# Kernel optimization log

Measured on AMD Instinct MI355X. Metric: run time of the kernel, lower is better.

Reference implementation:

```python
import math
import jax, jax.numpy as jnp
import numpy as np

PROB_SPARSE_FACTOR = 0.4


def setup_inputs() -> dict:
    key = jax.random.key(0)
    kq, kk, kv = jax.random.split(key, 3)
    B, H, T, S, D = 2, 16, 2048, 2048, 64
    q = jax.random.normal(kq, (B, H, T, D), dtype=jnp.float32)
    k = jax.random.normal(kk, (B, H, S, D), dtype=jnp.float32)
    v = jax.random.normal(kv, (B, H, S, D), dtype=jnp.float32)
    return {"q": q, "k": k, "v": v}


def reference(q, k, v):
    B, H, T, D = q.shape
    S = k.shape[2]
    scaling = 1.0 / math.sqrt(D)
    # Informer-style top-u query count (static, derived from shapes)
    u = max(int(min(PROB_SPARSE_FACTOR * math.log(S), T * 0.5)), int(T * 0.3))

    # KLD scoring over full attention approximation: [B,H,T,S]
    attn_approx = jnp.einsum("bhtd,bhsd->bhts", q * scaling, k)
    attn_approx = jnp.clip(attn_approx, -50.0, 50.0)
    attn_approx = attn_approx - jnp.max(attn_approx, axis=-1, keepdims=True)
    sm = jax.nn.softmax(attn_approx, axis=-1)
    log_uniform = math.log(S)
    kl_score = jnp.sum(sm * (jnp.log(sm + 1e-10) + log_uniform), axis=-1)  # [B,H,T]

    # Select top-u most informative queries per (b,h)
    _, topk_idx = jax.lax.top_k(kl_score, u)  # [B,H,u]

    # Sparse attention only for selected queries
    q_red = jnp.take_along_axis(q, topk_idx[..., None], axis=2)  # [B,H,u,D]
    scores = jnp.einsum("bhud,bhsd->bhus", q_red, k) * scaling
    scores = jnp.clip(scores, -50.0, 50.0)
    scores = scores - jnp.max(scores, axis=-1, keepdims=True)
    w = jax.nn.softmax(scores, axis=-1)
    w = jnp.clip(w, 1e-9, 1.0)
    out_red = jnp.einsum("bhus,bhsd->bhud", w, v)  # [B,H,u,D]

    # Scatter reduced outputs back into a zero-initialized full output
    b_i = jnp.arange(B)[:, None, None]
    h_i = jnp.arange(H)[None, :, None]
    out = jnp.zeros_like(q).at[b_i, h_i, topk_idx].set(out_red)
    return out
```

## Files before the change

kernel.cpp:

```cpp
#include <hip/hip_runtime.h>
#include <math.h>

#define T_DIM 2048
#define S_DIM 2048
#define D_DIM 64
#define BH_DIM 32
#define U_SEL 614
#define QROWS 48
#define LOG_S_D 7.624618986159398
#define LOG2E_F 1.4426950408889634f
#define LN2_D 0.6931471805599453
#define SCL_Q (0.125f * LOG2E_F)

typedef __attribute__((ext_vector_type(8))) short bf16x8;
typedef __attribute__((ext_vector_type(4))) short bf16x4;
typedef __attribute__((ext_vector_type(4))) float f32x4;

__device__ __forceinline__ unsigned short bf16_rne(float x) {
  unsigned u = __float_as_uint(x);
  u += 0x7FFF + ((u >> 16) & 1);
  return (unsigned short)(u >> 16);
}
__device__ __forceinline__ float bf16_to_f(unsigned short h) {
  return __uint_as_float(((unsigned)h) << 16);
}
#if defined(__has_builtin)
#if __has_builtin(__builtin_amdgcn_exp2f)
#define EXP2_HW(x) __builtin_amdgcn_exp2f(x)
#endif
#endif
#ifndef EXP2_HW
#define EXP2_HW(x) exp2f(x)
#endif

#define GLD_LDS16(g, l)                                                        \
  __builtin_amdgcn_global_load_lds(                                            \
      (const __attribute__((address_space(1))) unsigned int*)(const void*)(g), \
      (__attribute__((address_space(3))) unsigned int*)(void*)(l), 16, 0, 0)

__device__ __forceinline__ void stage_img16(const unsigned short* __restrict__ g,
                                            unsigned short* l, int lane, int w) {
#pragma unroll
  for (int it = 0; it < 4; ++it) {
    const int chunk = it * 4 + w;
    GLD_LDS16((const char*)g + chunk * 1024 + lane * 16, (char*)l + chunk * 1024);
  }
}
__device__ __forceinline__ void stage_img8(const unsigned short* __restrict__ g,
                                           unsigned short* l, int lane, int w) {
#pragma unroll
  for (int it = 0; it < 2; ++it) {
    const int chunk = it * 4 + w;
    GLD_LDS16((const char*)g + chunk * 1024 + lane * 16, (char*)l + chunk * 1024);
  }
}

__device__ __forceinline__ bf16x8 ldfrag_sw(const unsigned short* buf, int row, int chunk) {
  return *(const bf16x8*)(buf + (row << 6) + (((chunk) ^ (row & 7)) << 3));
}
__device__ __forceinline__ bf16x8 ldfrag_k128(const unsigned short* buf, int row, int chunk) {
  return *(const bf16x8*)(buf + ((row >> 6) << 12) + ((row & 63) << 6) +
                          (((chunk) ^ (row & 7)) << 3));
}

__global__ __launch_bounds__(256) void convert_kernel(
    const float* __restrict__ kin, const float* __restrict__ vin,
    const float* __restrict__ qin, unsigned short* __restrict__ kimg,
    unsigned short* __restrict__ vt_g, unsigned short* __restrict__ qimg,
    float* __restrict__ out) {
  __shared__ float vld[128][65];
  const int jb = blockIdx.x;
  const int tid = threadIdx.x;
  if (jb < 2048) {
    const bool isq = jb >= 1024;
    const int jj = jb & 1023;
    const int bh = jj >> 5, tl = jj & 31;
    const float* src = (isq ? qin : kin) + ((size_t)bh * 2048 + tl * 64) * 64;
    unsigned short* dst = (isq ? qimg : kimg) + (size_t)(bh * 32 + tl) * 8192;
    const float scl = isq ? SCL_Q : 1.0f;
#pragma unroll
    for (int g = 0; g < 2; ++g) {
      const int flat = g * 256 + tid;
      const int r = flat >> 3, c = flat & 7;
      const float4 f0 = *(const float4*)(src + r * 64 + c * 8);
      const float4 f1 = *(const float4*)(src + r * 64 + c * 8 + 4);
      const float xs[8] = {f0.x, f0.y, f0.z, f0.w, f1.x, f1.y, f1.z, f1.w};
      bf16x8 hv, lv;
#pragma unroll
      for (int j = 0; j < 8; ++j) {
        const float x = xs[j] * scl;
        const unsigned short h = bf16_rne(x);
        hv[j] = (short)h;
        lv[j] = (short)bf16_rne(x - bf16_to_f(h));
      }
      const int base = (r << 6) + ((c ^ (r & 7)) << 3);
      *(bf16x8*)(dst + base) = hv;
      *(bf16x8*)(dst + 4096 + base) = lv;
    }
  } else if (jb < 2560) {
    const int jv = jb - 2048;
    const int bh = jv >> 4, tl = jv & 15;
    const float* src = vin + ((size_t)bh * 2048 + tl * 128) * 64;
#pragma unroll
    for (int g = 0; g < 8; ++g) {
      const int f = g * 256 + tid;
      const int r = f >> 4, c4 = f & 15;
      const float4 x = *(const float4*)(src + r * 64 + c4 * 4);
      vld[r][c4 * 4 + 0] = x.x;
      vld[r][c4 * 4 + 1] = x.y;
      vld[r][c4 * 4 + 2] = x.z;
      vld[r][c4 * 4 + 3] = x.w;
    }
    __syncthreads();
    unsigned short* dst = vt_g + (size_t)(bh * 16 + tl) * 8192;
#pragma unroll
    for (int g = 0; g < 4; ++g) {
      const int oc = g * 256 + tid;
      const int d = oc >> 4, cc = oc & 15;
      bf16x8 hv;
#pragma unroll
      for (int j = 0; j < 8; ++j) hv[j] = (short)bf16_rne(vld[cc * 8 + j][d]);
      *(bf16x8*)(dst + (d << 7) + (((cc ^ (d & 15))) << 3)) = hv;
    }
  } else {
    float4* o4 = (float4*)out;
    const size_t b = (size_t)(jb - 2560);
#pragma unroll
    for (int g = 0; g < 8; ++g)
      o4[b * 2048 + g * 256 + tid] = make_float4(0.f, 0.f, 0.f, 0.f);
  }
}

__global__ __launch_bounds__(256, 2) void kl_score_mfma(
    const unsigned short* __restrict__ qimg, const unsigned short* __restrict__ kimg,
    float2* __restrict__ zw) {
  __shared__ __align__(16) unsigned short lbuf[2][8192];
  const int b = blockIdx.x;
  const int bh = b & 31;
  const int tt = (b >> 5) & 15;
  const int shalf = b >> 9;
  const int tid = threadIdx.x;
  const int lane = tid & 63, w = tid >> 6, quad = lane >> 4, l15 = lane & 15;
  const unsigned short* qb = qimg + (size_t)(bh * 32 + tt * 2) * 8192;
  const unsigned short* kb = kimg + (size_t)bh * (32 * 8192);
  const int tg0 = shalf * 16;

  stage_img16(qb, &lbuf[0][0], lane, w);
  stage_img16(qb + 8192, &lbuf[1][0], lane, w);
  __syncthreads();

  bf16x8 ah[2][2], al[2][2];
#pragma unroll
  for (int rt = 0; rt < 2; ++rt) {
    const int row = w * 32 + rt * 16 + l15;
    const unsigned short* lb = &lbuf[row >> 6][0];
    const int r64 = row & 63;
#pragma unroll
    for (int kc = 0; kc < 2; ++kc) {
      const int off = (r64 << 6) + (((kc * 4 + quad) ^ (r64 & 7)) << 3);
      ah[rt][kc] = *(const bf16x8*)(lb + off);
      al[rt][kc] = *(const bf16x8*)(lb + 4096 + off);
    }
  }
  __syncthreads();

  stage_img16(kb + (size_t)tg0 * 8192, &lbuf[0][0], lane, w);
  __syncthreads();

  float Zf[8], Wf[8];
#pragma unroll
  for (int i = 0; i < 8; ++i) { Zf[i] = 0.f; Wf[i] = 0.f; }

  for (int t = 0; t < 16; ++t) {
    if (t < 15)
      stage_img16(kb + (size_t)(tg0 + t + 1) * 8192, &lbuf[(t + 1) & 1][0], lane, w);
    const unsigned short* cb = &lbuf[t & 1][0];

    f32x4 acc[2][4];
#pragma unroll
    for (int rt = 0; rt < 2; ++rt)
#pragma unroll
      for (int ct = 0; ct < 4; ++ct) acc[rt][ct] = (f32x4){0.f, 0.f, 0.f, 0.f};

#pragma unroll
    for (int ct = 0; ct < 4; ++ct) {
      const int srow = ct * 16 + l15;
      const bf16x8 bh0 = ldfrag_sw(cb, srow, quad);
      const bf16x8 bl0 = ldfrag_sw(cb + 4096, srow, quad);
      const bf16x8 bh1 = ldfrag_sw(cb, srow, 4 + quad);
      const bf16x8 bl1 = ldfrag_sw(cb + 4096, srow, 4 + quad);
#pragma unroll
      for (int rt = 0; rt < 2; ++rt) {
        f32x4 c = acc[rt][ct];
        c = __builtin_amdgcn_mfma_f32_16x16x32_bf16(ah[rt][0], bh0, c, 0, 0, 0);
        c = __builtin_amdgcn_mfma_f32_16x16x32_bf16(al[rt][0], bh0, c, 0, 0, 0);
        c = __builtin_amdgcn_mfma_f32_16x16x32_bf16(ah[rt][0], bl0, c, 0, 0, 0);
        c = __builtin_amdgcn_mfma_f32_16x16x32_bf16(ah[rt][1], bh1, c, 0, 0, 0);
        c = __builtin_amdgcn_mfma_f32_16x16x32_bf16(al[rt][1], bh1, c, 0, 0, 0);
        c = __builtin_amdgcn_mfma_f32_16x16x32_bf16(ah[rt][1], bl1, c, 0, 0, 0);
        acc[rt][ct] = c;
      }
    }

#pragma unroll
    for (int rt = 0; rt < 2; ++rt)
#pragma unroll
      for (int r = 0; r < 4; ++r) {
        float zp = 0.f, wp = 0.f;
#pragma unroll
        for (int ct = 0; ct < 4; ++ct) {
          const float tv = acc[rt][ct][r];
          const float e = EXP2_HW(tv);
          zp += e;
          wp = fmaf(e, tv, wp);
        }
        Zf[rt * 4 + r] += zp;
        Wf[rt * 4 + r] += wp;
      }
    __syncthreads();
  }

#pragma unroll
  for (int i = 0; i < 8; ++i) {
    float Zt = Zf[i], Wt = Wf[i];
#pragma unroll
    for (int mask = 1; mask <= 8; mask <<= 1) {
      Zt += __shfl_xor(Zt, mask);
      Wt += __shfl_xor(Wt, mask);
    }
    if (l15 == 0) {
      const int row = tt * 128 + w * 32 + (i >> 2) * 16 + quad * 4 + (i & 3);
      zw[((size_t)shalf * 32 + bh) * 2048 + row] = make_float2(Zt, Wt);
    }
  }
}

__global__ __launch_bounds__(1024) void topk_kernel(const float2* __restrict__ zw,
                                                    int* __restrict__ topk) {
  __shared__ float sv[2048];
  __shared__ int si[2048];
  const int bh = blockIdx.x;
  const int tid = threadIdx.x;
  for (int i = tid; i < 2048; i += 1024) {
    const float2 a = zw[(size_t)bh * 2048 + i];
    const float2 c = zw[(size_t)(32 + bh) * 2048 + i];
    const double Z = (double)a.x + (double)c.x;
    const double W = (double)a.y + (double)c.y;
    sv[i] = (float)(LN2_D * (W / Z) - log(Z) + LOG_S_D);
    si[i] = i;
  }
  __syncthreads();
  for (int kk = 2; kk <= 2048; kk <<= 1) {
    for (int j = kk >> 1; j > 0; j >>= 1) {
      const int p = tid;
      const int i = ((p & ~(j - 1)) << 1) | (p & (j - 1));
      const int pr = i | j;
      const float v1 = sv[i], v2 = sv[pr];
      const int i1 = si[i], i2 = si[pr];
      const bool beforePI = (v2 > v1) || (v2 == v1 && i2 < i1);
      const bool dirDesc = ((i & kk) == 0);
      const bool doSwap = dirDesc ? beforePI : !beforePI;
      if (doSwap) { sv[i] = v2; sv[pr] = v1; si[i] = i2; si[pr] = i1; }
      __syncthreads();
    }
  }
  for (int i = tid; i < U_SEL; i += 1024) topk[bh * U_SEL + i] = si[i];
}

struct __align__(16) SmC {
  union { unsigned short kt[2][8192]; float obuf[QROWS * 64]; } a;
  union { unsigned short vt[2][8192]; float zred[4][QROWS]; } b;
  union { unsigned short qs[QROWS * 64]; unsigned short ps[4][QROWS * 40]; } c;
};

__global__ __launch_bounds__(256, 2) void sparse_attn_mfma(
    const float* __restrict__ q, const unsigned short* __restrict__ kimg,
    const unsigned short* __restrict__ vt_g, const int* __restrict__ topk,
    float* __restrict__ out) {
  __shared__ SmC sm;
  const int b = blockIdx.x;
  const int bh = b & 31;
  const int l0 = (b >> 5) * QROWS;
  const int tid = threadIdx.x;
  const int lane = tid & 63, w = tid >> 6, quad = lane >> 4, l15 = lane & 15;
  const float* qb = q + (size_t)bh * (2048 * 64);
  const unsigned short* kb = kimg + (size_t)bh * (32 * 8192);
  const unsigned short* vtb = vt_g + (size_t)bh * (16 * 8192);
  const int* tkb = topk + bh * U_SEL;

  {
#pragma unroll
    for (int g = 0; g < 2; ++g) {
      const int ch = g * 256 + tid;
      if (ch < QROWS * 8) {
        const int r = ch >> 3, c = ch & 7;
        const int l = l0 + r;
        const int row = (l < U_SEL) ? tkb[l] : tkb[0];
        const float4 f0 = *(const float4*)(qb + (size_t)row * 64 + c * 8);
        const float4 f1 = *(const float4*)(qb + (size_t)row * 64 + c * 8 + 4);
        const float xs[8] = {f0.x, f0.y, f0.z, f0.w, f1.x, f1.y, f1.z, f1.w};
        bf16x8 hv;
#pragma unroll
        for (int j = 0; j < 8; ++j) hv[j] = (short)bf16_rne(xs[j] * SCL_Q);
        *(bf16x8*)&sm.c.qs[(r << 6) + ((c ^ (r & 7)) << 3)] = hv;
      }
    }
  }
  stage_img8(kb, sm.a.kt[0], lane, w);
  stage_img8(kb + 8192, sm.a.kt[0] + 4096, lane, w);
  stage_img16(vtb, sm.b.vt[0], lane, w);
  __syncthreads();

  bf16x8 qf[3][2];
#pragma unroll
  for (int nt = 0; nt < 3; ++nt)
#pragma unroll
    for (int kc = 0; kc < 2; ++kc)
      qf[nt][kc] = ldfrag_sw(sm.c.qs, nt * 16 + l15, kc * 4 + quad);
  __syncthreads();

  float zrun[3] = {0.f, 0.f, 0.f};
  f32x4 oacc[3][4];
#pragma unroll
  for (int a = 0; a < 3; ++a)
#pragma unroll
    for (int b2 = 0; b2 < 4; ++b2) oacc[a][b2] = (f32x4){0.f, 0.f, 0.f, 0.f};

  for (int st = 0; st < 16; ++st) {
    if (st < 15) {
      unsigned short* kd = sm.a.kt[(st + 1) & 1];
      unsigned short* vd = sm.b.vt[(st + 1) & 1];
      stage_img8(kb + (size_t)(2 * st + 2) * 8192, kd, lane, w);
      stage_img8(kb + (size_t)(2 * st + 3) * 8192, kd + 4096, lane, w);
      stage_img16(vtb + (size_t)(st + 1) * 8192, vd, lane, w);
    }
    const unsigned short* kcur = sm.a.kt[st & 1];
    const unsigned short* vcur = sm.b.vt[st & 1];

    const int ar0 = w * 32 + l15, ar1 = w * 32 + 16 + l15;
    const bf16x8 a00 = ldfrag_k128(kcur, ar0, quad);
    const bf16x8 a01 = ldfrag_k128(kcur, ar0, 4 + quad);
    const bf16x8 a10 = ldfrag_k128(kcur, ar1, quad);
    const bf16x8 a11 = ldfrag_k128(kcur, ar1, 4 + quad);

    f32x4 sacc[2][3];
    __builtin_amdgcn_s_setprio(1);
#pragma unroll
    for (int mt = 0; mt < 2; ++mt)
#pragma unroll
      for (int nt = 0; nt < 3; ++nt) {
        f32x4 c = (f32x4){0.f, 0.f, 0.f, 0.f};
        c = __builtin_amdgcn_mfma_f32_16x16x32_bf16(mt ? a10 : a00, qf[nt][0], c, 0, 0, 0);
        c = __builtin_amdgcn_mfma_f32_16x16x32_bf16(mt ? a11 : a01, qf[nt][1], c, 0, 0, 0);
        sacc[mt][nt] = c;
      }
    __builtin_amdgcn_s_setprio(0);

#pragma unroll
    for (int nt = 0; nt < 3; ++nt) {
      float zl = 0.f;
#pragma unroll
      for (int mt = 0; mt < 2; ++mt) {
        bf16x4 pw;
#pragma unroll
        for (int r = 0; r < 4; ++r) {
          const float p = EXP2_HW(sacc[mt][nt][r]);
          zl += p;
          pw[r] = (short)bf16_rne(p);
        }
        *(bf16x4*)&sm.c.ps[w][(nt * 16 + l15) * 40 + mt * 16 + quad * 4] = pw;
      }
      zrun[nt] += zl;
    }

    bf16x8 vbf[4];
#pragma unroll
    for (int dt = 0; dt < 4; ++dt) {
      const int d = dt * 16 + l15;
      vbf[dt] = *(const bf16x8*)&vcur[(d << 7) + (((w * 4 + quad) ^ l15) << 3)];
    }

    __builtin_amdgcn_s_setprio(1);
#pragma unroll
    for (int mtq = 0; mtq < 3; ++mtq) {
      const bf16x8 pa = *(const bf16x8*)&sm.c.ps[w][(mtq * 16 + l15) * 40 + quad * 8];
#pragma unroll
      for (int dt = 0; dt < 4; ++dt)
        oacc[mtq][dt] = __builtin_amdgcn_mfma_f32_16x16x32_bf16(pa, vbf[dt], oacc[mtq][dt], 0, 0, 0);
    }
    __builtin_amdgcn_s_setprio(0);
    __syncthreads();
  }

#pragma unroll
  for (int nt = 0; nt < 3; ++nt) {
    float z = zrun[nt];
    z += __shfl_xor(z, 16);
    z += __shfl_xor(z, 32);
    if (quad == 0) sm.b.zred[w][nt * 16 + l15] = z;
  }
  for (int i = tid; i < QROWS * 64; i += 256) sm.a.obuf[i] = 0.f;
  __syncthreads();
#pragma unroll
  for (int mtq = 0; mtq < 3; ++mtq)
#pragma unroll
    for (int r = 0; r < 4; ++r) {
      const int qr = mtq * 16 + quad * 4 + r;
#pragma unroll
      for (int dt = 0; dt < 4; ++dt)
        atomicAdd(&sm.a.obuf[qr * 64 + dt * 16 + l15], oacc[mtq][dt][r]);
    }
  __syncthreads();
  {
    if (tid < QROWS * 4) {
      const int qr = tid >> 2, seg = tid & 3;
      const int l = l0 + qr;
      if (l < U_SEL) {
        const float Zt = sm.b.zred[0][qr] + sm.b.zred[1][qr] +
                         sm.b.zred[2][qr] + sm.b.zred[3][qr];
        const float inv = 1.0f / Zt;
        const int row = tkb[l];
        float* op = &out[((size_t)bh * T_DIM + row) * 64 + seg * 16];
        const float* ob = &sm.a.obuf[qr * 64 + seg * 16];
#pragma unroll
        for (int j = 0; j < 4; ++j) {
          float4 o;
          o.x = ob[j * 4 + 0] * inv;
          o.y = ob[j * 4 + 1] * inv;
          o.z = ob[j * 4 + 2] * inv;
          o.w = ob[j * 4 + 3] * inv;
          *(float4*)&op[j * 4] = o;
        }
      }
    }
  }
}

extern "C" void kernel_launch(void* const* d_in, const int* in_sizes, int n_in,
                              void* d_out, int out_size, void* d_ws, size_t ws_size,
                              hipStream_t stream) {
  const float* q = (const float*)d_in[0];
  const float* k = (const float*)d_in[1];
  const float* v = (const float*)d_in[2];
  float* out = (float*)d_out;
  char* ws = (char*)d_ws;
  float2* zw = (float2*)ws;
  int* topk = (int*)(ws + 1048576);
  unsigned short* kimg = (unsigned short*)(ws + 1310720);
  unsigned short* vt_g = (unsigned short*)(ws + 18087936);
  unsigned short* qimg = (unsigned short*)(ws + 26476544);

  convert_kernel<<<dim3(3072), dim3(256), 0, stream>>>(k, v, q, kimg, vt_g, qimg, out);
  kl_score_mfma<<<dim3(1024), dim3(256), 0, stream>>>(qimg, kimg, zw);
  topk_kernel<<<dim3(BH_DIM), dim3(1024), 0, stream>>>(zw, topk);
  sparse_attn_mfma<<<dim3(512), dim3(256), 0, stream>>>(q, kimg, vt_g, topk, out);
}
```

Before: 225.7 us.

## Load V fragments directly from global in MFMA order, shrink query tile

The convert kernel now writes V^T in an image laid out in per-lane MFMA fragment order. The sparse attention kernel can then load V operands straight from global memory into registers instead of staging them through LDS. Dropping the V LDS buffers frees shared memory, which allows a smaller 32-row query tile, 768 blocks, and launch bounds of 3 blocks per SM. In exchange, K tiles are reloaded more often across the larger block count, and the V loads are no longer double-buffered, so their latency may be exposed.

```diff
diff --git a/kernel.cpp b/kernel.cpp
--- a/kernel.cpp
+++ b/kernel.cpp
@@ -6,7 +6,7 @@
 #define D_DIM 64
 #define BH_DIM 32
 #define U_SEL 614
-#define QROWS 48
+#define QROWS 32
 #define LOG_S_D 7.624618986159398
 #define LOG2E_F 1.4426950408889634f
 #define LN2_D 0.6931471805599453
@@ -116,11 +116,12 @@
 #pragma unroll
     for (int g = 0; g < 4; ++g) {
       const int oc = g * 256 + tid;
-      const int d = oc >> 4, cc = oc & 15;
+      const int w4 = oc >> 8, dt = (oc >> 6) & 3, qd = (oc >> 4) & 3, l = oc & 15;
       bf16x8 hv;
 #pragma unroll
-      for (int j = 0; j < 8; ++j) hv[j] = (short)bf16_rne(vld[cc * 8 + j][d]);
-      *(bf16x8*)(dst + (d << 7) + (((cc ^ (d & 15))) << 3)) = hv;
+      for (int j = 0; j < 8; ++j)
+        hv[j] = (short)bf16_rne(vld[w4 * 32 + qd * 8 + j][dt * 16 + l]);
+      *(bf16x8*)(dst + oc * 8) = hv;
     }
   } else {
     float4* o4 = (float4*)out;
@@ -268,12 +269,14 @@
 }
 
 struct __align__(16) SmC {
-  union { unsigned short kt[2][8192]; float obuf[QROWS * 64]; } a;
-  union { unsigned short vt[2][8192]; float zred[4][QROWS]; } b;
+  union {
+    unsigned short kt[2][8192];
+    struct { float obuf[QROWS * 64]; float zred[4][QROWS]; } o;
+  } a;
   union { unsigned short qs[QROWS * 64]; unsigned short ps[4][QROWS * 40]; } c;
 };
 
-__global__ __launch_bounds__(256, 2) void sparse_attn_mfma(
+__global__ __launch_bounds__(256, 3) void sparse_attn_mfma(
     const float* __restrict__ q, const unsigned short* __restrict__ kimg,
     const unsigned short* __restrict__ vt_g, const int* __restrict__ topk,
     float* __restrict__ out) {
@@ -289,53 +292,50 @@
   const int* tkb = topk + bh * U_SEL;
 
   {
-#pragma unroll
-    for (int g = 0; g < 2; ++g) {
-      const int ch = g * 256 + tid;
-      if (ch < QROWS * 8) {
-        const int r = ch >> 3, c = ch & 7;
-        const int l = l0 + r;
-        const int row = (l < U_SEL) ? tkb[l] : tkb[0];
-        const float4 f0 = *(const float4*)(qb + (size_t)row * 64 + c * 8);
-        const float4 f1 = *(const float4*)(qb + (size_t)row * 64 + c * 8 + 4);
-        const float xs[8] = {f0.x, f0.y, f0.z, f0.w, f1.x, f1.y, f1.z, f1.w};
-        bf16x8 hv;
-#pragma unroll
-        for (int j = 0; j < 8; ++j) hv[j] = (short)bf16_rne(xs[j] * SCL_Q);
-        *(bf16x8*)&sm.c.qs[(r << 6) + ((c ^ (r & 7)) << 3)] = hv;
-      }
-    }
+    const int ch = tid;
+    const int r = ch >> 3, c = ch & 7;
+    const int l = l0 + r;
+    const int row = (l < U_SEL) ? tkb[l] : tkb[0];
+    const float4 f0 = *(const float4*)(qb + (size_t)row * 64 + c * 8);
+    const float4 f1 = *(const float4*)(qb + (size_t)row * 64 + c * 8 + 4);
+    const float xs[8] = {f0.x, f0.y, f0.z, f0.w, f1.x, f1.y, f1.z, f1.w};
+    bf16x8 hv;
+#pragma unroll
+    for (int j = 0; j < 8; ++j) hv[j] = (short)bf16_rne(xs[j] * SCL_Q);
+    *(bf16x8*)&sm.c.qs[(r << 6) + ((c ^ (r & 7)) << 3)] = hv;
   }
   stage_img8(kb, sm.a.kt[0], lane, w);
   stage_img8(kb + 8192, sm.a.kt[0] + 4096, lane, w);
-  stage_img16(vtb, sm.b.vt[0], lane, w);
-  __syncthreads();
-
-  bf16x8 qf[3][2];
-#pragma unroll
-  for (int nt = 0; nt < 3; ++nt)
+  __syncthreads();
+
+  bf16x8 qf[2][2];
+#pragma unroll
+  for (int nt = 0; nt < 2; ++nt)
 #pragma unroll
     for (int kc = 0; kc < 2; ++kc)
       qf[nt][kc] = ldfrag_sw(sm.c.qs, nt * 16 + l15, kc * 4 + quad);
   __syncthreads();
 
-  float zrun[3] = {0.f, 0.f, 0.f};
-  f32x4 oacc[3][4];
-#pragma unroll
-  for (int a = 0; a < 3; ++a)
+  float zrun[2] = {0.f, 0.f};
+  f32x4 oacc[2][4];
+#pragma unroll
+  for (int a = 0; a < 2; ++a)
 #pragma unroll
     for (int b2 = 0; b2 < 4; ++b2) oacc[a][b2] = (f32x4){0.f, 0.f, 0.f, 0.f};
 
   for (int st = 0; st < 16; ++st) {
     if (st < 15) {
       unsigned short* kd = sm.a.kt[(st + 1) & 1];
-      unsigned short* vd = sm.b.vt[(st + 1) & 1];
       stage_img8(kb + (size_t)(2 * st + 2) * 8192, kd, lane, w);
       stage_img8(kb + (size_t)(2 * st + 3) * 8192, kd + 4096, lane, w);
-      stage_img16(vtb + (size_t)(st + 1) * 8192, vd, lane, w);
-    }
+    }
+    const char* vp = (const char*)(vtb + (size_t)st * 8192);
+    bf16x8 vbf[4];
+#pragma unroll
+    for (int dt = 0; dt < 4; ++dt)
+      vbf[dt] = *(const bf16x8*)(vp + w * 4096 + dt * 1024 + lane * 16);
+
     const unsigned short* kcur = sm.a.kt[st & 1];
-    const unsigned short* vcur = sm.b.vt[st & 1];
 
     const int ar0 = w * 32 + l15, ar1 = w * 32 + 16 + l15;
     const bf16x8 a00 = ldfrag_k128(kcur, ar0, quad);
@@ -343,12 +343,12 @@
     const bf16x8 a10 = ldfrag_k128(kcur, ar1, quad);
     const bf16x8 a11 = ldfrag_k128(kcur, ar1, 4 + quad);
 
-    f32x4 sacc[2][3];
+    f32x4 sacc[2][2];
     __builtin_amdgcn_s_setprio(1);
 #pragma unroll
     for (int mt = 0; mt < 2; ++mt)
 #pragma unroll
-      for (int nt = 0; nt < 3; ++nt) {
+      for (int nt = 0; nt < 2; ++nt) {
         f32x4 c = (f32x4){0.f, 0.f, 0.f, 0.f};
         c = __builtin_amdgcn_mfma_f32_16x16x32_bf16(mt ? a10 : a00, qf[nt][0], c, 0, 0, 0);
         c = __builtin_amdgcn_mfma_f32_16x16x32_bf16(mt ? a11 : a01, qf[nt][1], c, 0, 0, 0);
@@ -357,7 +357,7 @@
     __builtin_amdgcn_s_setprio(0);
 
 #pragma unroll
-    for (int nt = 0; nt < 3; ++nt) {
+    for (int nt = 0; nt < 2; ++nt) {
       float zl = 0.f;
 #pragma unroll
       for (int mt = 0; mt < 2; ++mt) {
@@ -373,16 +373,9 @@
       zrun[nt] += zl;
     }
 
-    bf16x8 vbf[4];
-#pragma unroll
-    for (int dt = 0; dt < 4; ++dt) {
-      const int d = dt * 16 + l15;
-      vbf[dt] = *(const bf16x8*)&vcur[(d << 7) + (((w * 4 + quad) ^ l15) << 3)];
-    }
-
     __builtin_amdgcn_s_setprio(1);
 #pragma unroll
-    for (int mtq = 0; mtq < 3; ++mtq) {
+    for (int mtq = 0; mtq < 2; ++mtq) {
       const bf16x8 pa = *(const bf16x8*)&sm.c.ps[w][(mtq * 16 + l15) * 40 + quad * 8];
 #pragma unroll
       for (int dt = 0; dt < 4; ++dt)
@@ -393,22 +386,22 @@
   }
 
 #pragma unroll
-  for (int nt = 0; nt < 3; ++nt) {
+  for (int nt = 0; nt < 2; ++nt) {
     float z = zrun[nt];
     z += __shfl_xor(z, 16);
     z += __shfl_xor(z, 32);
-    if (quad == 0) sm.b.zred[w][nt * 16 + l15] = z;
-  }
-  for (int i = tid; i < QROWS * 64; i += 256) sm.a.obuf[i] = 0.f;
-  __syncthreads();
-#pragma unroll
-  for (int mtq = 0; mtq < 3; ++mtq)
+    if (quad == 0) sm.a.o.zred[w][nt * 16 + l15] = z;
+  }
+  for (int i = tid; i < QROWS * 64; i += 256) sm.a.o.obuf[i] = 0.f;
+  __syncthreads();
+#pragma unroll
+  for (int mtq = 0; mtq < 2; ++mtq)
 #pragma unroll
     for (int r = 0; r < 4; ++r) {
       const int qr = mtq * 16 + quad * 4 + r;
 #pragma unroll
       for (int dt = 0; dt < 4; ++dt)
-        atomicAdd(&sm.a.obuf[qr * 64 + dt * 16 + l15], oacc[mtq][dt][r]);
+        atomicAdd(&sm.a.o.obuf[qr * 64 + dt * 16 + l15], oacc[mtq][dt][r]);
     }
   __syncthreads();
   {
@@ -416,12 +409,12 @@
       const int qr = tid >> 2, seg = tid & 3;
       const int l = l0 + qr;
       if (l < U_SEL) {
-        const float Zt = sm.b.zred[0][qr] + sm.b.zred[1][qr] +
-                         sm.b.zred[2][qr] + sm.b.zred[3][qr];
+        const float Zt = sm.a.o.zred[0][qr] + sm.a.o.zred[1][qr] +
+                         sm.a.o.zred[2][qr] + sm.a.o.zred[3][qr];
         const float inv = 1.0f / Zt;
         const int row = tkb[l];
         float* op = &out[((size_t)bh * T_DIM + row) * 64 + seg * 16];
-        const float* ob = &sm.a.obuf[qr * 64 + seg * 16];
+        const float* ob = &sm.a.o.obuf[qr * 64 + seg * 16];
 #pragma unroll
         for (int j = 0; j < 4; ++j) {
           float4 o;
@@ -453,5 +446,5 @@
   convert_kernel<<<dim3(3072), dim3(256), 0, stream>>>(k, v, q, kimg, vt_g, qimg, out);
   kl_score_mfma<<<dim3(1024), dim3(256), 0, stream>>>(qimg, kimg, zw);
   topk_kernel<<<dim3(BH_DIM), dim3(1024), 0, stream>>>(zw, topk);
-  sparse_attn_mfma<<<dim3(512), dim3(256), 0, stream>>>(q, kimg, vt_g, topk, out);
-}
+  sparse_attn_mfma<<<dim3(768), dim3(256), 0, stream>>>(q, kimg, vt_g, topk, out);
+}
```

After: 220.2 us. 1.02x faster.
